# Performance work log

Measured on AMD Instinct MI355X. Metric: run time of the kernel, lower is better.

The kernel has to match this reference:

```python
import jax, jax.numpy as jnp
import numpy as np

B, C, K = 128, 32, 128


def setup_inputs() -> dict:
    key = jax.random.key(0)
    k1, k2, k3, k4, k5 = jax.random.split(key, 5)
    x = jax.random.normal(k1, (B, 1, K, K), dtype=jnp.float32)
    # Conv2d(1, C, (1, K)) weight -> effectively [C, K] over the column axis
    w_col = jax.random.normal(k2, (C, K), dtype=jnp.float32) * (1.0 / np.sqrt(K))
    b_col = jax.random.normal(k3, (C,), dtype=jnp.float32) * 0.01
    # Conv2d(1, C, (K, 1)) weight -> effectively [C, K] over the row axis
    w_row = jax.random.normal(k4, (C, K), dtype=jnp.float32) * (1.0 / np.sqrt(K))
    b_row = jax.random.normal(k5, (C,), dtype=jnp.float32) * 0.01
    return {"x": x, "w_col": w_col, "b_col": b_col, "w_row": w_row, "b_row": b_row}


def reference(x, w_col, b_col, w_row, b_row):
    xs = x[:, 0]  # [B, K, K]
    # conv_column: kernel (1, K) contracts the column axis j -> [B, C, K] (rows i)
    col = jnp.einsum("bij,cj->bci", xs, w_col) + b_col[None, :, None]
    # conv_row: kernel (K, 1) contracts the row axis i -> [B, C, K] (cols j)
    row = jnp.einsum("bij,ci->bcj", xs, w_row) + b_row[None, :, None]
    # Tiling conv_row to [B,C,K,K] (identical rows) and conv_column to
    # [B,C,K,K] (identical columns) and matmul-ing yields, for every (i, j):
    #   out[b,c,i,j] = sum_k row[b,c,k] * col[b,c,k]
    # i.e. a per-(b,c) scalar broadcast over the K x K plane.
    s = jnp.einsum("bck,bck->bc", row, col)  # [B, C]
    return jnp.broadcast_to(s[:, :, None, None], (x.shape[0], w_col.shape[0], K, K))
```

## Files before the change

### kernel.cpp

```cpp
#include <hip/hip_runtime.h>
#include <hip/hip_bf16.h>


constexpr int KDIM = 128;
constexpr int CDIM = 32;

__global__ __launch_bounds__(512) void fused_kernel(
    const float* __restrict__ x,
    const float* __restrict__ w_col, const float* __restrict__ b_col,
    const float* __restrict__ w_row, const float* __restrict__ b_row,
    float* __restrict__ out)
{
    __shared__ __align__(16) float xs[KDIM * KDIM];
    __shared__ float4 wu4[KDIM][4];
    __shared__ float4 wcv[16][32];
    __shared__ __align__(16) float uvx[2 * 16 * KDIM];

    const int bid  = blockIdx.x;
    const int xcd  = bid & 7;
    const int idx  = bid >> 3;
    const int b    = xcd * 16 + (idx >> 1);
    const int ch   = idx & 1;
    const int C0   = ch * 16;
    const int tid  = threadIdx.x;
    const int w    = tid >> 6;
    const int lane = tid & 63;

    const float* xg = x + (size_t)b * KDIM * KDIM;
    {
        const int cb = w * 64 + lane;
        #pragma unroll
        for (int e = 0; e < 8; ++e) {
            const int c    = cb + 512 * e;
            const int row  = c >> 5;
            const int scol = (c & 31) ^ ((c >> 7) & 31);
            __builtin_amdgcn_global_load_lds(
                (const __attribute__((address_space(1))) unsigned int*)(xg + row * KDIM + 4 * scol),
                (__attribute__((address_space(3))) unsigned int*)(&xs[4 * c]),
                16, 0, 0);
        }
    }
    {
        const int i = tid & 127;
        const int g = tid >> 7;
        wu4[i][g] = make_float4(w_row[(C0 + 4 * g + 0) * KDIM + i],
                                w_row[(C0 + 4 * g + 1) * KDIM + i],
                                w_row[(C0 + 4 * g + 2) * KDIM + i],
                                w_row[(C0 + 4 * g + 3) * KDIM + i]);
        const int c16 = tid >> 5;
        const int jc  = tid & 31;
        wcv[c16][jc] = *reinterpret_cast<const float4*>(&w_col[(C0 + c16) * KDIM + 4 * jc]);
    }
    __syncthreads();

    const int role = w >> 2;
    const int g    = w & 3;
    const int kq   = lane & 31;
    const int ih   = lane >> 5;

    float a[4][4] = {{0,0,0,0},{0,0,0,0},{0,0,0,0},{0,0,0,0}};

    if (role == 0) {
        #pragma unroll 4
        for (int ii = 0; ii < 64; ++ii) {
            const int i     = ih * 64 + ii;
            const int chunk = kq ^ ((i >> 2) & 31);
            const float4 xv = *reinterpret_cast<const float4*>(&xs[i * KDIM + 4 * chunk]);
            const float4 wq = wu4[i][g];
            #pragma unroll
            for (int cc = 0; cc < 4; ++cc) {
                const float ww = (&wq.x)[cc];
                a[cc][0] = fmaf(ww, xv.x, a[cc][0]);
                a[cc][1] = fmaf(ww, xv.y, a[cc][1]);
                a[cc][2] = fmaf(ww, xv.z, a[cc][2]);
                a[cc][3] = fmaf(ww, xv.w, a[cc][3]);
            }
        }
    } else {
        #pragma unroll 2
        for (int jj = 0; jj < 16; ++jj) {
            const int jcol = ih * 16 + jj;
            float4 tv[4];
            #pragma unroll
            for (int r = 0; r < 4; ++r) {
                const int row   = 4 * kq + r;
                const int chunk = jcol ^ kq;
                tv[r] = *reinterpret_cast<const float4*>(&xs[row * KDIM + 4 * chunk]);
            }
            #pragma unroll
            for (int cc = 0; cc < 4; ++cc) {
                const float4 wq = wcv[4 * g + cc][jcol];
                #pragma unroll
                for (int r = 0; r < 4; ++r) {
                    a[cc][r] = fmaf(wq.x, tv[r].x, a[cc][r]);
                    a[cc][r] = fmaf(wq.y, tv[r].y, a[cc][r]);
                    a[cc][r] = fmaf(wq.z, tv[r].z, a[cc][r]);
                    a[cc][r] = fmaf(wq.w, tv[r].w, a[cc][r]);
                }
            }
        }
    }

    #pragma unroll
    for (int cc = 0; cc < 4; ++cc)
        #pragma unroll
        for (int q = 0; q < 4; ++q)
            a[cc][q] += __shfl_xor(a[cc][q], 32);

    if (lane < 32) {
        float* ex = uvx + role * 2048;
        #pragma unroll
        for (int cc = 0; cc < 4; ++cc) {
            *reinterpret_cast<float4*>(&ex[(4 * g + cc) * KDIM + 4 * kq]) =
                make_float4(a[cc][0], a[cc][1], a[cc][2], a[cc][3]);
        }
    }
    __syncthreads();

    {
        const int cg  = tid >> 5;
        const int kq2 = tid & 31;
        const float4 uu = *reinterpret_cast<const float4*>(&uvx[cg * KDIM + 4 * kq2]);
        const float4 vv = *reinterpret_cast<const float4*>(&uvx[2048 + cg * KDIM + 4 * kq2]);
        const int c = C0 + cg;
        const float br = b_row[c];
        const float bc = b_col[c];
        float p = (uu.x + br) * (vv.x + bc) + (uu.y + br) * (vv.y + bc)
                + (uu.z + br) * (vv.z + bc) + (uu.w + br) * (vv.w + bc);
        #pragma unroll
        for (int off = 1; off < 32; off <<= 1) p += __shfl_xor(p, off, 32);
        float4 v4;
        v4.x = v4.y = v4.z = v4.w = p;
        float4* o = reinterpret_cast<float4*>(out) + (size_t)(b * CDIM + c) * 4096;
        #pragma unroll 8
        for (int r = 0; r < 128; ++r) {
            o[kq2 + 32 * r] = v4;
        }
    }
}

extern "C" void kernel_launch(void* const* d_in, const int* in_sizes, int n_in,
                              void* d_out, int out_size, void* d_ws, size_t ws_size,
                              hipStream_t stream) {
    const float* x     = (const float*)d_in[0];
    const float* w_col = (const float*)d_in[1];
    const float* b_col = (const float*)d_in[2];
    const float* w_row = (const float*)d_in[3];
    const float* b_row = (const float*)d_in[4];
    float* out = (float*)d_out;

    fused_kernel<<<256, 512, 0, stream>>>(x, w_col, b_col, w_row, b_row, out);
}
```

Baseline: 50.96 us.

## Split channels into four groups of eight to double the block count

```diff
diff --git a/kernel.cpp b/kernel.cpp
--- a/kernel.cpp
+++ b/kernel.cpp
@@ -5,23 +5,23 @@
 constexpr int KDIM = 128;
 constexpr int CDIM = 32;
 
-__global__ __launch_bounds__(512) void fused_kernel(
+__global__ __launch_bounds__(512, 4) void fused_kernel(
     const float* __restrict__ x,
     const float* __restrict__ w_col, const float* __restrict__ b_col,
     const float* __restrict__ w_row, const float* __restrict__ b_row,
     float* __restrict__ out)
 {
     __shared__ __align__(16) float xs[KDIM * KDIM];
-    __shared__ float4 wu4[KDIM][4];
-    __shared__ float4 wcv[16][32];
-    __shared__ __align__(16) float uvx[2 * 16 * KDIM];
+    __shared__ float2 wu2[KDIM][4];
+    __shared__ float4 wcv[8][32];
+    __shared__ __align__(16) float uvx[2 * 8 * KDIM];
 
     const int bid  = blockIdx.x;
     const int xcd  = bid & 7;
     const int idx  = bid >> 3;
-    const int b    = xcd * 16 + (idx >> 1);
-    const int ch   = idx & 1;
-    const int C0   = ch * 16;
+    const int b    = xcd * 16 + (idx >> 2);
+    const int oct  = idx & 3;
+    const int C0   = oct * 8;
     const int tid  = threadIdx.x;
     const int w    = tid >> 6;
     const int lane = tid & 63;
@@ -40,16 +40,18 @@
                 16, 0, 0);
         }
     }
-    {
+    if (tid < 256) {
         const int i = tid & 127;
-        const int g = tid >> 7;
-        wu4[i][g] = make_float4(w_row[(C0 + 4 * g + 0) * KDIM + i],
-                                w_row[(C0 + 4 * g + 1) * KDIM + i],
-                                w_row[(C0 + 4 * g + 2) * KDIM + i],
-                                w_row[(C0 + 4 * g + 3) * KDIM + i]);
-        const int c16 = tid >> 5;
-        const int jc  = tid & 31;
-        wcv[c16][jc] = *reinterpret_cast<const float4*>(&w_col[(C0 + c16) * KDIM + 4 * jc]);
+        const int g = (tid >> 7) * 2;
+        wu2[i][g]     = make_float2(w_row[(C0 + 2 * g + 0) * KDIM + i],
+                                    w_row[(C0 + 2 * g + 1) * KDIM + i]);
+        wu2[i][g + 1] = make_float2(w_row[(C0 + 2 * g + 2) * KDIM + i],
+                                    w_row[(C0 + 2 * g + 3) * KDIM + i]);
+    } else {
+        const int t  = tid - 256;
+        const int c8 = t >> 5;
+        const int jc = t & 31;
+        wcv[c8][jc] = *reinterpret_cast<const float4*>(&w_col[(C0 + c8) * KDIM + 4 * jc]);
     }
     __syncthreads();
 
@@ -58,7 +60,7 @@
     const int kq   = lane & 31;
     const int ih   = lane >> 5;
 
-    float a[4][4] = {{0,0,0,0},{0,0,0,0},{0,0,0,0},{0,0,0,0}};
+    float a[2][4] = {{0,0,0,0},{0,0,0,0}};
 
     if (role == 0) {
         #pragma unroll 4
@@ -66,15 +68,11 @@
             const int i     = ih * 64 + ii;
             const int chunk = kq ^ ((i >> 2) & 31);
             const float4 xv = *reinterpret_cast<const float4*>(&xs[i * KDIM + 4 * chunk]);
-            const float4 wq = wu4[i][g];
-            #pragma unroll
-            for (int cc = 0; cc < 4; ++cc) {
-                const float ww = (&wq.x)[cc];
-                a[cc][0] = fmaf(ww, xv.x, a[cc][0]);
-                a[cc][1] = fmaf(ww, xv.y, a[cc][1]);
-                a[cc][2] = fmaf(ww, xv.z, a[cc][2]);
-                a[cc][3] = fmaf(ww, xv.w, a[cc][3]);
-            }
+            const float2 wq = wu2[i][g];
+            a[0][0] = fmaf(wq.x, xv.x, a[0][0]); a[0][1] = fmaf(wq.x, xv.y, a[0][1]);
+            a[0][2] = fmaf(wq.x, xv.z, a[0][2]); a[0][3] = fmaf(wq.x, xv.w, a[0][3]);
+            a[1][0] = fmaf(wq.y, xv.x, a[1][0]); a[1][1] = fmaf(wq.y, xv.y, a[1][1]);
+            a[1][2] = fmaf(wq.y, xv.z, a[1][2]); a[1][3] = fmaf(wq.y, xv.w, a[1][3]);
         }
     } else {
         #pragma unroll 2
@@ -88,8 +86,8 @@
                 tv[r] = *reinterpret_cast<const float4*>(&xs[row * KDIM + 4 * chunk]);
             }
             #pragma unroll
-            for (int cc = 0; cc < 4; ++cc) {
-                const float4 wq = wcv[4 * g + cc][jcol];
+            for (int cc = 0; cc < 2; ++cc) {
+                const float4 wq = wcv[2 * g + cc][jcol];
                 #pragma unroll
                 for (int r = 0; r < 4; ++r) {
                     a[cc][r] = fmaf(wq.x, tv[r].x, a[cc][r]);
@@ -102,39 +100,36 @@
     }
 
     #pragma unroll
-    for (int cc = 0; cc < 4; ++cc)
+    for (int cc = 0; cc < 2; ++cc)
         #pragma unroll
         for (int q = 0; q < 4; ++q)
             a[cc][q] += __shfl_xor(a[cc][q], 32);
 
     if (lane < 32) {
-        float* ex = uvx + role * 2048;
+        float* ex = uvx + role * 1024;
         #pragma unroll
-        for (int cc = 0; cc < 4; ++cc) {
-            *reinterpret_cast<float4*>(&ex[(4 * g + cc) * KDIM + 4 * kq]) =
+        for (int cc = 0; cc < 2; ++cc) {
+            *reinterpret_cast<float4*>(&ex[(2 * g + cc) * KDIM + 4 * kq]) =
                 make_float4(a[cc][0], a[cc][1], a[cc][2], a[cc][3]);
         }
     }
     __syncthreads();
 
     {
-        const int cg  = tid >> 5;
-        const int kq2 = tid & 31;
-        const float4 uu = *reinterpret_cast<const float4*>(&uvx[cg * KDIM + 4 * kq2]);
-        const float4 vv = *reinterpret_cast<const float4*>(&uvx[2048 + cg * KDIM + 4 * kq2]);
-        const int c = C0 + cg;
+        const int c = C0 + w;
+        const float2 uu = *reinterpret_cast<const float2*>(&uvx[w * KDIM + 2 * lane]);
+        const float2 vv = *reinterpret_cast<const float2*>(&uvx[1024 + w * KDIM + 2 * lane]);
         const float br = b_row[c];
         const float bc = b_col[c];
-        float p = (uu.x + br) * (vv.x + bc) + (uu.y + br) * (vv.y + bc)
-                + (uu.z + br) * (vv.z + bc) + (uu.w + br) * (vv.w + bc);
+        float p = (uu.x + br) * (vv.x + bc) + (uu.y + br) * (vv.y + bc);
         #pragma unroll
-        for (int off = 1; off < 32; off <<= 1) p += __shfl_xor(p, off, 32);
+        for (int off = 1; off < 64; off <<= 1) p += __shfl_xor(p, off);
         float4 v4;
         v4.x = v4.y = v4.z = v4.w = p;
         float4* o = reinterpret_cast<float4*>(out) + (size_t)(b * CDIM + c) * 4096;
         #pragma unroll 8
-        for (int r = 0; r < 128; ++r) {
-            o[kq2 + 32 * r] = v4;
+        for (int r = 0; r < 64; ++r) {
+            o[lane + 64 * r] = v4;
         }
     }
 }
@@ -149,5 +144,5 @@
     const float* b_row = (const float*)d_in[4];
     float* out = (float*)d_out;
 
-    fused_kernel<<<256, 512, 0, stream>>>(x, w_col, b_col, w_row, b_row, out);
+    fused_kernel<<<512, 512, 0, stream>>>(x, w_col, b_col, w_row, b_row, out);
 }
```

Result: faster. 49.78 us (-2.3%).
